# Kernel tuning notes

Hardware: AMD Instinct MI355X
Metric: run time of the kernel (lower is better)

## Reference

```python
import jax, jax.numpy as jnp
import numpy as np

PAD = 0
B, S, D, H, NH, PF, V, NMAX, L = 32, 512, 256, 512, 8, 2048, 100000, 15, 2
HD = H // NH


def setup_inputs() -> dict:
    key = jax.random.key(0)
    ks = iter(jax.random.split(key, 40))
    N = B * S
    p = lambda *s: jax.random.normal(next(ks), s, dtype=jnp.float32) * 0.02
    return dict(
        src=jax.random.randint(next(ks), (B, S), 0, V),
        src_lengths=jax.random.randint(next(ks), (B,), 1, S + 1),
        neighbor_idx=jax.random.randint(next(ks), (N, NMAX), 0, N),
        neighbor_count=jax.random.randint(next(ks), (N,), 0, NMAX + 1),
        time_intervals=jax.random.uniform(next(ks), (B, S), dtype=jnp.float32),
        emb=p(V, D).at[PAD].set(0.0),
        time_W=p(D), time_b=p(D),
        soc_W=p(D, D), soc_b=p(D), soc_g=jnp.ones(D), soc_beta=jnp.zeros(D),
        proj_W=p(D, H), proj_b=p(H),
        Wq=p(L, H, H), bq=p(L, H), Wk=p(L, H, H), bk=p(L, H),
        Wv=p(L, H, H), bv=p(L, H), Wo=p(L, H, H), bo=p(L, H),
        ln1_g=jnp.ones((L, H)), ln1_b=jnp.zeros((L, H)),
        ff_W1=p(L, H, PF), ff_b1=p(L, PF), ff_W2=p(L, PF, H), ff_b2=p(L, H),
        ln2_g=jnp.ones((L, H)), ln2_b=jnp.zeros((L, H)),
    )


def _ln(x, g, b):
    mu = x.mean(-1, keepdims=True)
    v = ((x - mu) ** 2).mean(-1, keepdims=True)
    return (x - mu) / jnp.sqrt(v + 1e-5) * g + b


def _forward(src, neighbor_idx, neighbor_count, time_intervals, emb, time_W, time_b,
             soc_W, soc_b, soc_g, soc_beta, proj_W, proj_b,
             Wq, bq, Wk, bk, Wv, bv, Wo, bo, ln1_g, ln1_b,
             ff_W1, ff_b1, ff_W2, ff_b2, ln2_g, ln2_b):
    # embedding + sinusoidal positional encoding
    x = emb[src]  # [B,S,D]
    pos = jnp.arange(S, dtype=jnp.float32)[:, None]
    div = jnp.exp(jnp.arange(0, D, 2, dtype=jnp.float32) * (-np.log(10000.0) / D))
    pe = jnp.zeros((S, D)).at[:, 0::2].set(jnp.sin(pos * div)).at[:, 1::2].set(jnp.cos(pos * div))
    x = x + pe
    # time interval encoding: Linear(1, D) on t[...,None]
    x = x + time_intervals[..., None] * time_W + time_b
    # neighbor aggregation (batched form of the per-node loop: mean over <=15 valid neighbors)
    N = B * S
    flat = x.reshape(N, D)
    nb = flat[neighbor_idx]  # [N, NMAX, D] irregular gather
    m = (jnp.arange(NMAX)[None, :] < neighbor_count[:, None]).astype(flat.dtype)
    agg = (nb * m[..., None]).sum(1) / jnp.maximum(neighbor_count, 1).astype(flat.dtype)[:, None]
    soc = jax.nn.relu(_ln(flat + agg @ soc_W + soc_b, soc_g, soc_beta))
    soc = jnp.where((neighbor_count > 0)[:, None], soc, flat)  # no neighbors -> passthrough
    soc = jnp.where((src.reshape(N) != PAD)[:, None], soc, 0.0)  # only valid (non-PAD) tokens
    x = x + 0.2 * soc.reshape(B, S, D)
    # transformer encoder stack
    h = x @ proj_W + proj_b
    kmask = src != PAD  # [B,S]
    for l in range(L):
        q = (h @ Wq[l] + bq[l]).reshape(B, S, NH, HD)
        k = (h @ Wk[l] + bk[l]).reshape(B, S, NH, HD)
        v = (h @ Wv[l] + bv[l]).reshape(B, S, NH, HD)
        e = jnp.einsum('bqhd,bkhd->bhqk', q, k) / jnp.sqrt(jnp.float32(HD))
        e = jnp.where(kmask[:, None, None, :], e, -1e10)
        a = jax.nn.softmax(e, axis=-1)
        o = jnp.einsum('bhqk,bkhd->bqhd', a, v).reshape(B, S, H)
        h = _ln(h + o @ Wo[l] + bo[l], ln1_g[l], ln1_b[l])
        ff = jax.nn.relu(h @ ff_W1[l] + ff_b1[l]) @ ff_W2[l] + ff_b2[l]
        h = _ln(h + ff, ln2_g[l], ln2_b[l])
    return h, x  # (src_out, embedded)


def reference(src, src_lengths, neighbor_idx, neighbor_count, time_intervals, emb, time_W, time_b,
              soc_W, soc_b, soc_g, soc_beta, proj_W, proj_b,
              Wq, bq, Wk, bk, Wv, bv, Wo, bo, ln1_g, ln1_b,
              ff_W1, ff_b1, ff_W2, ff_b2, ln2_g, ln2_b):
    # src_lengths unused by the original forward
    return _forward(src, neighbor_idx, neighbor_count, time_intervals, emb, time_W, time_b,
                    soc_W, soc_b, soc_g, soc_beta, proj_W, proj_b,
                    Wq, bq, Wk, bk, Wv, bv, Wo, bo, ln1_g, ln1_b,
                    ff_W1, ff_b1, ff_W2, ff_b2, ln2_g, ln2_b)
```

## Files before the change

### kernel.cpp

```cpp
#include <hip/hip_runtime.h>

#define BB 32
#define SS 512
#define DD 256
#define HHH 512
#define NHH 8
#define HDD 64
#define PFF 2048
#define LLL 2
#define NN (BB*SS)
#define NMAXX 15

typedef unsigned short u16;
typedef unsigned int u32;

typedef __attribute__((ext_vector_type(8))) __bf16 bf16x8;
typedef __attribute__((ext_vector_type(4))) float f32x4;

__device__ __forceinline__ float bf2f(u16 u) {
  union { u32 i; float f; } x; x.i = ((u32)u) << 16; return x.f;
}
__device__ __forceinline__ u16 f2bf(float f) {
  union { float f; u32 i; } x; x.f = f;
  u32 r = x.i + 0x7FFFu + ((x.i >> 16) & 1u);
  return (u16)(r >> 16);
}
__device__ __forceinline__ float ldf(const void* p, size_t i, int flag) {
  return flag ? bf2f(((const u16*)p)[i]) : ((const float*)p)[i];
}
__device__ __forceinline__ void stf(void* p, size_t i, int flag, float v) {
  if (flag) ((u16*)p)[i] = f2bf(v); else ((float*)p)[i] = v;
}
__device__ __forceinline__ void gld16(const u16* g, u16* l) {
  __builtin_amdgcn_global_load_lds(
      (const __attribute__((address_space(1))) u32*)g,
      (__attribute__((address_space(3))) u32*)l, 16, 0, 0);
}

__global__ void k_flag(const u32* __restrict__ ones, int* __restrict__ flag) {
  *flag = (ones[0] == 0x3F800000u) ? 0 : 1;
}

__global__ __launch_bounds__(256) void k_transpose_f(const void* __restrict__ in, size_t ioff,
    u16* __restrict__ out, int R, int C, const int* __restrict__ flagp) {
  __shared__ u16 tile[32][33];
  int flag = *flagp;
  int c0 = blockIdx.x * 32, r0 = blockIdx.y * 32;
  int tx = threadIdx.x, ty = threadIdx.y;
  #pragma unroll
  for (int i = 0; i < 4; ++i)
    tile[ty + i*8][tx] = f2bf(ldf(in, ioff + (size_t)(r0 + ty + i*8) * C + c0 + tx, flag));
  __syncthreads();
  #pragma unroll
  for (int i = 0; i < 4; ++i) out[(size_t)(c0 + ty + i*8) * R + r0 + tx] = tile[tx][ty + i*8];
}

__global__ __launch_bounds__(256) void k_packb(const void* __restrict__ projb,
    const void* __restrict__ bq, const void* __restrict__ bk, const void* __restrict__ bv,
    const void* __restrict__ b1, const void* __restrict__ bo, const void* __restrict__ b2,
    u16* __restrict__ out, const int* __restrict__ flagp) {
  int flag = *flagp;
  int i = blockIdx.x * 256 + threadIdx.x;
  int tot = 512 + LLL * 4608;
  if (i >= tot) return;
  float v;
  if (i < 512) v = ldf(projb, i, flag);
  else {
    int j = i - 512, l = j / 4608, r = j % 4608;
    if      (r < 512)  v = ldf(bq, (size_t)l * HHH + r, flag);
    else if (r < 1024) v = ldf(bk, (size_t)l * HHH + r - 512, flag);
    else if (r < 1536) v = ldf(bv, (size_t)l * HHH + r - 1024, flag);
    else if (r < 3584) v = ldf(b1, (size_t)l * PFF + r - 1536, flag);
    else if (r < 4096) v = ldf(bo, (size_t)l * HHH + r - 3584, flag);
    else               v = ldf(b2, (size_t)l * HHH + r - 4096, flag);
  }
  out[i] = f2bf(v);
}

__global__ __launch_bounds__(256) void k_pe(const void* __restrict__ tB,
    u16* __restrict__ pet, const int* __restrict__ flagp) {
  int flag = *flagp;
  int s = blockIdx.x, d = threadIdx.x;
  int i2 = d & ~1;
  float freq = expf(-0.035977892078031968f * (float)i2);
  float ang = (float)s * freq;
  float v = ((d & 1) ? cosf(ang) : sinf(ang)) + ldf(tB, d, flag);
  pet[(size_t)s * DD + d] = f2bf(v);
}

__global__ __launch_bounds__(256) void k_embed(const int* __restrict__ src,
    const void* __restrict__ tiv, const void* __restrict__ emb,
    const void* __restrict__ tW, const u16* __restrict__ pet,
    u16* __restrict__ X, const int* __restrict__ flagp) {
  int flag = *flagp;
  int n = blockIdx.x, d = threadIdx.x;
  int s = n & (SS - 1);
  int tok = src[n];
  float v = ldf(emb, (size_t)tok * DD + d, flag);
  v += bf2f(pet[(size_t)s * DD + d]);
  float t = ldf(tiv, n, flag);
  v += t * ldf(tW, d, flag);
  X[(size_t)n * DD + d] = f2bf(v);
}

__global__ __launch_bounds__(256) void k_agg(const int* __restrict__ nidx,
    const int* __restrict__ ncnt, const u16* __restrict__ X, u16* __restrict__ AGG) {
  int n = blockIdx.x, d = threadIdx.x;
  int cnt = ncnt[n];
  float s = 0.f;
  for (int j = 0; j < cnt; ++j) {
    int m = nidx[n * NMAXX + j];
    s += bf2f(X[(size_t)m * DD + d]);
  }
  float div = (float)(cnt > 0 ? cnt : 1);
  AGG[(size_t)n * DD + d] = f2bf(s / div);
}

__global__ __launch_bounds__(256) void k_gemm128(const u16* __restrict__ A,
    const u16* __restrict__ BT, const void* __restrict__ bias, int boff,
    const u16* __restrict__ res, u16* __restrict__ C, int N, int K, int relu,
    const int* __restrict__ flagp) {
  __shared__ __align__(16) u16 As[128 * 32];
  __shared__ __align__(16) u16 Bs[128 * 32];
  int n0 = blockIdx.x * 128, m0 = blockIdx.y * 128;
  int t = threadIdx.x;
  int lane = t & 63, w = t >> 6;
  int wm = (w >> 1) * 64, wn = (w & 1) * 64;
  int fr = lane & 15, fq = lane >> 4;
  int srow = t >> 2, sseg = t & 3;

  f32x4 acc[4][4];
  #pragma unroll
  for (int i = 0; i < 4; ++i)
    #pragma unroll
    for (int j = 0; j < 4; ++j) acc[i][j] = (f32x4){0.f, 0.f, 0.f, 0.f};

  const u16* ga = A  + (size_t)(m0 + srow) * K + sseg * 8;
  const u16* gb = BT + (size_t)(n0 + srow) * K + sseg * 8;
  u16* lA = As + srow * 32 + sseg * 8;
  u16* lB = Bs + srow * 32 + sseg * 8;
  const size_t rstride = (size_t)64 * K;

  for (int k0 = 0; k0 < K; k0 += 32) {
    gld16(ga + k0, lA);
    gld16(ga + k0 + rstride, lA + 64 * 32);
    gld16(gb + k0, lB);
    gld16(gb + k0 + rstride, lB + 64 * 32);
    __syncthreads();
    bf16x8 af[4], bf[4];
    #pragma unroll
    for (int i = 0; i < 4; ++i) af[i] = *(const bf16x8*)&As[(wm + i * 16 + fr) * 32 + fq * 8];
    #pragma unroll
    for (int j = 0; j < 4; ++j) bf[j] = *(const bf16x8*)&Bs[(wn + j * 16 + fr) * 32 + fq * 8];
    #pragma unroll
    for (int i = 0; i < 4; ++i)
      #pragma unroll
      for (int j = 0; j < 4; ++j)
        acc[i][j] = __builtin_amdgcn_mfma_f32_16x16x32_bf16(af[i], bf[j], acc[i][j], 0, 0, 0);
    __syncthreads();
  }

  int flag = *flagp;
  #pragma unroll
  for (int j = 0; j < 4; ++j) {
    int col = n0 + wn + j * 16 + fr;
    float bv = bias ? ldf(bias, boff + col, flag) : 0.f;
    #pragma unroll
    for (int i = 0; i < 4; ++i) {
      #pragma unroll
      for (int c = 0; c < 4; ++c) {
        int row = m0 + wm + i * 16 + fq * 4 + c;
        float v = acc[i][j][c] + bv;
        if (res) v += bf2f(res[(size_t)row * N + col]);
        if (relu) v = fmaxf(v, 0.f);
        C[(size_t)row * N + col] = f2bf(v);
      }
    }
  }
}

template<int NBF>
__global__ __launch_bounds__(512, 2) void k_gemm256(const u16* __restrict__ A,
    const u16* __restrict__ BT, const u16* __restrict__ bias,
    u16* __restrict__ C, int N, int K, int relu, int nbx) {
  constexpr int AG = 1024;
  constexpr int BG = NBF * 256;
  constexpr int STRIDE = (AG + BG) * 8;
  constexpr int LPT = 2 + BG / 512;
  __shared__ __align__(16) u16 S[3 * STRIDE];

  int nwg = gridDim.x;
  int id = blockIdx.x;
  int wg = ((nwg & 7) == 0) ? ((id & 7) * (nwg >> 3) + (id >> 3)) : id;
  int bx = wg % nbx, by = wg / nbx;
  int m0 = by * 256, n0 = bx * (64 * NBF);

  int t = threadIdx.x;
  int w = t >> 6, lane = t & 63;
  int fr = lane & 15, fq = lane >> 4;
  int wm = (w >> 2) * 128, wn = (w & 3) * (16 * NBF);
  int gsw8 = (fq ^ (fr & 3) ^ ((fr >> 2) & 3)) * 8;

  int arow = t >> 2, aseg = t & 3;
  int asw = aseg ^ (arow & 3) ^ ((arow >> 2) & 3);
  const u16* gA  = A  + (size_t)(m0 + arow) * K + asw * 8;
  const u16* gA2 = gA + (size_t)128 * K;
  const u16* gB  = BT + (size_t)(n0 + arow) * K + asw * 8;
  const u16* gB2 = gB + (size_t)128 * K;

  f32x4 acc[8][NBF];
  #pragma unroll
  for (int i = 0; i < 8; ++i)
    #pragma unroll
    for (int j = 0; j < NBF; ++j) acc[i][j] = (f32x4){0.f, 0.f, 0.f, 0.f};

  int NT = K >> 5;

  #pragma unroll
  for (int p = 0; p < 2; ++p) {
    gld16(gA  + p * 32, S + p * STRIDE + t * 8);
    gld16(gA2 + p * 32, S + p * STRIDE + (t + 512) * 8);
    gld16(gB  + p * 32, S + p * STRIDE + AG * 8 + t * 8);
    if constexpr (NBF == 4)
      gld16(gB2 + p * 32, S + p * STRIDE + AG * 8 + (t + 512) * 8);
  }
  asm volatile("s_waitcnt vmcnt(%0)" :: "n"(LPT) : "memory");
  __builtin_amdgcn_s_barrier();
  __builtin_amdgcn_sched_barrier(0);

  for (int T = 0; T < NT; ++T) {
    const u16* Sa = S + (T % 3) * STRIDE;
    const u16* Sb = Sa + AG * 8;
    u16* Sn = S + ((T + 2) % 3) * STRIDE;
    int kn = (T + 2) * 32;
    bool st = (T + 2) < NT;

    bf16x8 af[4], bf[NBF];
    #pragma unroll
    for (int i = 0; i < 4; ++i) af[i] = *(const bf16x8*)&Sa[(wm + i * 16 + fr) * 32 + gsw8];
    #pragma unroll
    for (int j = 0; j < NBF; ++j) bf[j] = *(const bf16x8*)&Sb[(wn + j * 16 + fr) * 32 + gsw8];
    if (st) {
      gld16(gA  + kn, Sn + t * 8);
      gld16(gA2 + kn, Sn + (t + 512) * 8);
    }
    __builtin_amdgcn_s_setprio(1);
    #pragma unroll
    for (int i = 0; i < 4; ++i)
      #pragma unroll
      for (int j = 0; j < NBF; ++j)
        acc[i][j] = __builtin_amdgcn_mfma_f32_16x16x32_bf16(af[i], bf[j], acc[i][j], 0, 0, 0);
    __builtin_amdgcn_s_setprio(0);

    bf16x8 ag[4];
    #pragma unroll
    for (int i = 0; i < 4; ++i) ag[i] = *(const bf16x8*)&Sa[(wm + 64 + i * 16 + fr) * 32 + gsw8];
    if (st) {
      gld16(gB + kn, Sn + AG * 8 + t * 8);
      if constexpr (NBF == 4)
        gld16(gB2 + kn, Sn + AG * 8 + (t + 512) * 8);
    }
    __builtin_amdgcn_s_setprio(1);
    #pragma unroll
    for (int i = 0; i < 4; ++i)
      #pragma unroll
      for (int j = 0; j < NBF; ++j)
        acc[4 + i][j] = __builtin_amdgcn_mfma_f32_16x16x32_bf16(ag[i], bf[j], acc[4 + i][j], 0, 0, 0);
    __builtin_amdgcn_s_setprio(0);

    if (st) { asm volatile("s_waitcnt vmcnt(%0) lgkmcnt(0)" :: "n"(LPT) : "memory"); }
    else    { asm volatile("s_waitcnt vmcnt(0) lgkmcnt(0)" ::: "memory"); }
    __builtin_amdgcn_s_barrier();
    __builtin_amdgcn_sched_barrier(0);
  }

  float bvj[NBF];
  #pragma unroll
  for (int j = 0; j < NBF; ++j) bvj[j] = bf2f(bias[n0 + wn + j * 16 + fr]);
  #pragma unroll
  for (int i = 0; i < 8; ++i) {
    #pragma unroll
    for (int c = 0; c < 4; ++c) {
      size_t rowb = (size_t)(m0 + wm + i * 16 + fq * 4 + c) * N;
      #pragma unroll
      for (int j = 0; j < NBF; ++j) {
        int col = n0 + wn + j * 16 + fr;
        float v = acc[i][j][c] + bvj[j];
        if (relu) v = fmaxf(v, 0.f);
        C[rowb + col] = f2bf(v);
      }
    }
  }
}

__global__ __launch_bounds__(256) void k_ln_soc(const u16* __restrict__ socp,
    const u16* __restrict__ X, const void* __restrict__ g, const void* __restrict__ beta,
    const int* __restrict__ ncnt, const int* __restrict__ src,
    u16* __restrict__ X2, void* __restrict__ dout, const int* __restrict__ flagp) {
  __shared__ float sred[4];
  int flag = *flagp;
  int n = blockIdx.x, t = threadIdx.x;
  size_t base = (size_t)n * DD;
  float v = bf2f(socp[base + t]);
  float s = v;
  #pragma unroll
  for (int o = 32; o; o >>= 1) s += __shfl_xor(s, o, 64);
  if ((t & 63) == 0) sred[t >> 6] = s;
  __syncthreads();
  float mean = (sred[0] + sred[1] + sred[2] + sred[3]) * (1.f / DD);
  float dv = v - mean;
  float q = dv * dv;
  #pragma unroll
  for (int o = 32; o; o >>= 1) q += __shfl_xor(q, o, 64);
  __syncthreads();
  if ((t & 63) == 0) sred[t >> 6] = q;
  __syncthreads();
  float var = (sred[0] + sred[1] + sred[2] + sred[3]) * (1.f / DD);
  float rs = rsqrtf(var + 1e-5f);
  float soc = fmaxf(dv * rs * ldf(g, t, flag) + ldf(beta, t, flag), 0.f);
  float xv = bf2f(X[base + t]);
  if (ncnt[n] <= 0) soc = xv;
  if (src[n] == 0)  soc = 0.f;
  float ov = xv + 0.2f * soc;
  X2[base + t] = f2bf(ov);
  stf(dout, (size_t)NN * HHH + base + t, flag, ov);
}

__global__ __launch_bounds__(256) void k_ln_add(const u16* __restrict__ a,
    const u16* __restrict__ b, const void* __restrict__ g, int goff,
    const void* __restrict__ bb, int boff, u16* __restrict__ out,
    void* __restrict__ dout, const int* __restrict__ flagp) {
  __shared__ float sred[4];
  int flag = *flagp;
  int row = blockIdx.x, t = threadIdx.x;
  size_t base = (size_t)row * HHH;
  float v0 = bf2f(a[base + t])       + bf2f(b[base + t]);
  float v1 = bf2f(a[base + 256 + t]) + bf2f(b[base + 256 + t]);
  float s = v0 + v1;
  #pragma unroll
  for (int o = 32; o; o >>= 1) s += __shfl_xor(s, o, 64);
  if ((t & 63) == 0) sred[t >> 6] = s;
  __syncthreads();
  float mean = (sred[0] + sred[1] + sred[2] + sred[3]) * (1.f / HHH);
  float d0 = v0 - mean, d1 = v1 - mean;
  float q = d0 * d0 + d1 * d1;
  #pragma unroll
  for (int o = 32; o; o >>= 1) q += __shfl_xor(q, o, 64);
  __syncthreads();
  if ((t & 63) == 0) sred[t >> 6] = q;
  __syncthreads();
  float var = (sred[0] + sred[1] + sred[2] + sred[3]) * (1.f / HHH);
  float rs = rsqrtf(var + 1e-5f);
  float o0 = d0 * rs * ldf(g, goff + t, flag)       + ldf(bb, boff + t, flag);
  float o1 = d1 * rs * ldf(g, goff + 256 + t, flag) + ldf(bb, boff + 256 + t, flag);
  if (dout) {
    stf(dout, base + t, flag, o0);
    stf(dout, base + 256 + t, flag, o1);
  } else {
    out[base + t]       = f2bf(o0);
    out[base + 256 + t] = f2bf(o1);
  }
}

__global__ __launch_bounds__(512, 2) void k_attn_mfma(const u16* __restrict__ Q,
    const u16* __restrict__ Kb, const u16* __restrict__ Vb, int ld,
    const int* __restrict__ src, u16* __restrict__ O) {
  __shared__ __align__(16) u16 Ks[512 * 64];
  __shared__ __align__(16) u16 VTs[64 * 512];
  __shared__ __align__(16) u16 Ps[128 * 72];
  __shared__ float maskv[512];
  int h = blockIdx.x, b = blockIdx.y;
  int t = threadIdx.x;
  int w = t >> 6, lane = t & 63;
  int fr = lane & 15, fq = lane >> 4;

  maskv[t] = (src[b * SS + t] != 0) ? 1.f : 0.f;

  #pragma unroll
  for (int i = 0; i < 8; ++i) {
    int off = t + i * 512;
    int row = off >> 3;
    int gs  = (off & 7) ^ (row & 7);
    gld16(Kb + (size_t)(b * SS + row) * ld + h * HDD + gs * 8, Ks + (size_t)off * 8);
  }
  {
    const u16* vsrc = Vb + (size_t)(b * SS + t) * ld + h * HDD;
    int ghi = (t >> 3) & ~7, glo = (t >> 3) & 7, kw = t & 7;
    #pragma unroll
    for (int i = 0; i < 8; ++i) {
      uint4 raw = *(const uint4*)(vsrc + i * 8);
      u16 e[8]; *(uint4*)e = raw;
      #pragma unroll
      for (int jj = 0; jj < 8; ++jj) {
        int d = i * 8 + jj;
        VTs[(size_t)d * 512 + (size_t)((ghi | (glo ^ (d & 7))) * 8 + kw)] = e[jj];
      }
    }
  }
  __syncthreads();

  for (int chunk = 0; chunk < 4; ++chunk) {
    int qb = chunk * 128 + w * 16;
    bf16x8 qf[2];
    #pragma unroll
    for (int kc = 0; kc < 2; ++kc)
      qf[kc] = *(const bf16x8*)&Q[(size_t)(b * SS + qb + fr) * ld + h * HDD + kc * 32 + fq * 8];

    f32x4 sacc[32];
    #pragma unroll
    for (int j = 0; j < 32; ++j) sacc[j] = (f32x4){0.f, 0.f, 0.f, 0.f};

    #pragma unroll
    for (int kt = 0; kt < 32; ++kt) {
      int row = kt * 16 + fr;
      #pragma unroll
      for (int kc = 0; kc < 2; ++kc) {
        bf16x8 kf = *(const bf16x8*)&Ks[(size_t)row * 64 +
            (size_t)(((kc * 4 + fq) ^ (fr & 7)) * 8)];
        sacc[kt] = __builtin_amdgcn_mfma_f32_16x16x32_bf16(qf[kc], kf, sacc[kt], 0, 0, 0);
      }
    }

    #pragma unroll
    for (int j = 0; j < 32; ++j) {
      float mv = maskv[j * 16 + fr];
      #pragma unroll
      for (int c = 0; c < 4; ++c) {
        float v = sacc[j][c] * 0.125f;
        sacc[j][c] = (mv != 0.f) ? v : -1e10f;
      }
    }
    #pragma unroll
    for (int c = 0; c < 4; ++c) {
      float m = -3.0e38f;
      #pragma unroll
      for (int j = 0; j < 32; ++j) m = fmaxf(m, sacc[j][c]);
      #pragma unroll
      for (int o = 1; o < 16; o <<= 1) m = fmaxf(m, __shfl_xor(m, o, 64));
      float s = 0.f;
      #pragma unroll
      for (int j = 0; j < 32; ++j) { float e = __expf(sacc[j][c] - m); sacc[j][c] = e; s += e; }
      #pragma unroll
      for (int o = 1; o < 16; o <<= 1) s += __shfl_xor(s, o, 64);
      float inv = 1.f / s;
      #pragma unroll
      for (int j = 0; j < 32; ++j) sacc[j][c] *= inv;
    }

    f32x4 oacc[4];
    #pragma unroll
    for (int n = 0; n < 4; ++n) oacc[n] = (f32x4){0.f, 0.f, 0.f, 0.f};

    #pragma unroll
    for (int seg = 0; seg < 8; ++seg) {
      #pragma unroll
      for (int tt = 0; tt < 4; ++tt)
        #pragma unroll
        for (int c = 0; c < 4; ++c)
          Ps[(size_t)(w * 16 + fq * 4 + c) * 72 + tt * 16 + fr] = f2bf(sacc[seg * 4 + tt][c]);
      #pragma unroll
      for (int kc = 0; kc < 2; ++kc) {
        bf16x8 pa = *(const bf16x8*)&Ps[(size_t)(w * 16 + fr) * 72 + kc * 32 + fq * 8];
        #pragma unroll
        for (int nt = 0; nt < 4; ++nt) {
          bf16x8 bv = *(const bf16x8*)&VTs[(size_t)(nt * 16 + fr) * 512 +
              (size_t)((seg * 8 + ((kc * 4 + fq) ^ (fr & 7))) * 8)];
          oacc[nt] = __builtin_amdgcn_mfma_f32_16x16x32_bf16(pa, bv, oacc[nt], 0, 0, 0);
        }
      }
    }

    #pragma unroll
    for (int nt = 0; nt < 4; ++nt)
      #pragma unroll
      for (int c = 0; c < 4; ++c)
        O[(size_t)(b * SS + qb + fq * 4 + c) * HHH + h * HDD + nt * 16 + fr] = f2bf(oacc[nt][c]);
  }
}

extern "C" void kernel_launch(void* const* d_in, const int* in_sizes, int n_in,
                              void* d_out, int out_size, void* d_ws, size_t ws_size,
                              hipStream_t stream) {
  (void)in_sizes; (void)n_in; (void)out_size;
  const int* src    = (const int*)d_in[0];
  const int* nidx   = (const int*)d_in[2];
  const int* ncnt   = (const int*)d_in[3];
  const void* tiv   = d_in[4];
  const void* emb   = d_in[5];
  const void* tW    = d_in[6];
  const void* tB    = d_in[7];
  const void* socW  = d_in[8];
  const void* socb  = d_in[9];
  const void* socg  = d_in[10];
  const void* socbe = d_in[11];
  const void* projW = d_in[12];
  const void* projb = d_in[13];
  const void* Wq    = d_in[14];
  const void* bq    = d_in[15];
  const void* Wk    = d_in[16];
  const void* bk    = d_in[17];
  const void* Wv    = d_in[18];
  const void* bv    = d_in[19];
  const void* Wo    = d_in[20];
  const void* bo    = d_in[21];
  const void* ln1g  = d_in[22];
  const void* ln1b  = d_in[23];
  const void* W1    = d_in[24];
  const void* b1    = d_in[25];
  const void* W2    = d_in[26];
  const void* b2    = d_in[27];
  const void* ln2g  = d_in[28];
  const void* ln2b  = d_in[29];

  const size_t NHS = (size_t)NN * HHH;
  const size_t QKV3 = (size_t)3 * HHH * HHH;
  u16* ws = (u16*)d_ws;
  u16* socWT  = ws;
  u16* projWT = socWT + (size_t)DD * DD;
  u16* WqkvT  = projWT + (size_t)DD * HHH;
  u16* WoT    = WqkvT + (size_t)LLL * QKV3;
  u16* W1T    = WoT + (size_t)LLL * HHH * HHH;
  u16* W2T    = W1T + (size_t)LLL * HHH * PFF;
  u16* Hb     = W2T + (size_t)LLL * HHH * PFF;
  u16* P1     = Hb + NHS;
  u16* P2     = P1 + NHS;
  u16* P3     = P2 + NHS;
  int* flagp  = (int*)(P3 + NHS);
  u16* packb  = (u16*)(flagp + 4);
  u16* pet    = packb + 16384;
  u16* FFMf   = pet + (size_t)SS * DD;
  size_t need_full = (size_t)(FFMf - ws + (size_t)NN * PFF) * 2;
  int fullff = (ws_size >= need_full);

  u16* X    = P1;
  u16* AGG  = P2;
  u16* SOCP = P3;
  u16* X2   = P2;
  u16* Ob   = (u16*)d_out;
  u16* FFMc = P2;

  k_flag<<<1, 1, 0, stream>>>((const u32*)ln1g, flagp);

  dim3 tb(32, 8);
  k_transpose_f<<<dim3(DD / 32, DD / 32), tb, 0, stream>>>(socW, 0, socWT, DD, DD, flagp);
  k_transpose_f<<<dim3(HHH / 32, DD / 32), tb, 0, stream>>>(projW, 0, projWT, DD, HHH, flagp);
  for (int l = 0; l < LLL; ++l) {
    size_t oHH = (size_t)l * HHH * HHH, oHP = (size_t)l * HHH * PFF;
    u16* wq = WqkvT + (size_t)l * QKV3;
    k_transpose_f<<<dim3(HHH / 32, HHH / 32), tb, 0, stream>>>(Wq, oHH, wq, HHH, HHH, flagp);
    k_transpose_f<<<dim3(HHH / 32, HHH / 32), tb, 0, stream>>>(Wk, oHH, wq + (size_t)HHH * HHH, HHH, HHH, flagp);
    k_transpose_f<<<dim3(HHH / 32, HHH / 32), tb, 0, stream>>>(Wv, oHH, wq + (size_t)2 * HHH * HHH, HHH, HHH, flagp);
    k_transpose_f<<<dim3(HHH / 32, HHH / 32), tb, 0, stream>>>(Wo, oHH, WoT + oHH, HHH, HHH, flagp);
    k_transpose_f<<<dim3(PFF / 32, HHH / 32), tb, 0, stream>>>(W1, oHP, W1T + oHP, HHH, PFF, flagp);
    k_transpose_f<<<dim3(HHH / 32, PFF / 32), tb, 0, stream>>>(W2, oHP, W2T + oHP, PFF, HHH, flagp);
  }
  k_packb<<<dim3((512 + LLL * 4608 + 255) / 256), 256, 0, stream>>>(
      projb, bq, bk, bv, b1, bo, b2, packb, flagp);
  k_pe<<<SS, 256, 0, stream>>>(tB, pet, flagp);

  k_embed<<<NN, 256, 0, stream>>>(src, tiv, emb, tW, pet, X, flagp);
  k_agg<<<NN, 256, 0, stream>>>(nidx, ncnt, X, AGG);
  k_gemm128<<<dim3(DD / 128, NN / 128), 256, 0, stream>>>(AGG, socWT, socb, 0, X, SOCP, DD, DD, 0, flagp);
  k_ln_soc<<<NN, 256, 0, stream>>>(SOCP, X, socg, socbe, ncnt, src, X2, d_out, flagp);
  k_gemm256<2><<<dim3(256), 512, 0, stream>>>(X2, projWT, packb, Hb, HHH, DD, 0, 4);

  for (int l = 0; l < LLL; ++l) {
    size_t oHH = (size_t)l * HHH * HHH, oHP = (size_t)l * HHH * PFF;
    u16* lb = packb + 512 + (size_t)l * 4608;
    k_gemm256<4><<<dim3(384), 512, 0, stream>>>(Hb, WqkvT + (size_t)l * QKV3, lb, P1, 1536, HHH, 0, 6);
    k_attn_mfma<<<dim3(NHH, BB), 512, 0, stream>>>(P1, P1 + HHH, P1 + 2 * HHH, 3 * HHH, src, Ob);
    k_gemm256<2><<<dim3(256), 512, 0, stream>>>(Ob, WoT + oHH, lb + 3584, P1, HHH, HHH, 0, 4);
    k_ln_add<<<NN, 256, 0, stream>>>(Hb, P1, ln1g, l * HHH, ln1b, l * HHH, Hb, nullptr, flagp);
    if (fullff) {
      k_gemm256<4><<<dim3(512), 512, 0, stream>>>(Hb, W1T + oHP, lb + 1536, FFMf, PFF, HHH, 1, 8);
      k_gemm256<2><<<dim3(256), 512, 0, stream>>>(FFMf, W2T + oHP, lb + 4096, P1, HHH, PFF, 0, 4);
    } else {
      for (int c = 0; c < 2; ++c) {
        const u16* Asrc = Hb + (size_t)c * 8192 * HHH;
        u16* Cdst = P1 + (size_t)c * 8192 * HHH;
        k_gemm256<4><<<dim3(256), 512, 0, stream>>>(Asrc, W1T + oHP, lb + 1536, FFMc, PFF, HHH, 1, 8);
        k_gemm256<2><<<dim3(128), 512, 0, stream>>>(FFMc, W2T + oHP, lb + 4096, Cdst, HHH, PFF, 0, 4);
      }
    }
    void* dd = (l == LLL - 1) ? d_out : nullptr;
    k_ln_add<<<NN, 256, 0, stream>>>(Hb, P1, ln2g, l * HHH, ln2b, l * HHH, Hb, dd, flagp);
  }
}
```

Measured before the change: 804.5 us.

## Merge weight transposes into one launch and streamline attention softmax

The fourteen per-matrix transpose launches become one kernel that maps block IDs to the right weight matrix, cutting launch overhead. In attention, the MFMA operands are swapped so each lane holds scores for a full row segment. The mask becomes an additive bias loaded as a vector, and the max and sum reductions need two cross-lane shuffles instead of several per column. Normalisation is deferred to the output store, and P is packed to bf16 with v_cvt_pk_bf16_f32 using 8-byte LDS writes. The risk is subtle numerical differences from the additive mask and the deferred scaling.

```diff
diff --git a/kernel.cpp b/kernel.cpp
--- a/kernel.cpp
+++ b/kernel.cpp
@@ -41,11 +41,34 @@
   *flag = (ones[0] == 0x3F800000u) ? 0 : 1;
 }
 
-__global__ __launch_bounds__(256) void k_transpose_f(const void* __restrict__ in, size_t ioff,
-    u16* __restrict__ out, int R, int C, const int* __restrict__ flagp) {
+__global__ __launch_bounds__(256) void k_transpose_all(
+    const void* __restrict__ socW, const void* __restrict__ projW,
+    const void* __restrict__ Wq, const void* __restrict__ Wk,
+    const void* __restrict__ Wv, const void* __restrict__ Wo,
+    const void* __restrict__ W1, const void* __restrict__ W2,
+    u16* __restrict__ socWT, u16* __restrict__ projWT, u16* __restrict__ WqkvT,
+    u16* __restrict__ WoT, u16* __restrict__ W1T, u16* __restrict__ W2T,
+    const int* __restrict__ flagp) {
+  const size_t HH2 = (size_t)HHH * HHH, HP = (size_t)HHH * PFF;
+  int bid = blockIdx.x;
+  const void* in; size_t ioff; u16* out; int R, C;
+  if (bid < 64)       { in = socW;  ioff = 0; out = socWT;  R = DD; C = DD;  }
+  else if (bid < 192) { bid -= 64; in = projW; ioff = 0; out = projWT; R = DD; C = HHH; }
+  else {
+    int r = bid - 192;
+    int l = r / 3072; r -= l * 3072;
+    size_t oHH = (size_t)l * HH2, oHP = (size_t)l * HP;
+    if (r < 256)       { in = Wq; ioff = oHH; out = WqkvT + (size_t)l*3*HH2;          R = HHH; C = HHH; bid = r; }
+    else if (r < 512)  { in = Wk; ioff = oHH; out = WqkvT + (size_t)l*3*HH2 + HH2;    R = HHH; C = HHH; bid = r - 256; }
+    else if (r < 768)  { in = Wv; ioff = oHH; out = WqkvT + (size_t)l*3*HH2 + 2*HH2;  R = HHH; C = HHH; bid = r - 512; }
+    else if (r < 1024) { in = Wo; ioff = oHH; out = WoT + oHH;                        R = HHH; C = HHH; bid = r - 768; }
+    else if (r < 2048) { in = W1; ioff = oHP; out = W1T + oHP;                        R = HHH; C = PFF; bid = r - 1024; }
+    else               { in = W2; ioff = oHP; out = W2T + oHP;                        R = PFF; C = HHH; bid = r - 2048; }
+  }
+  int ntx = C >> 5;
+  int c0 = (bid % ntx) * 32, r0 = (bid / ntx) * 32;
   __shared__ u16 tile[32][33];
   int flag = *flagp;
-  int c0 = blockIdx.x * 32, r0 = blockIdx.y * 32;
   int tx = threadIdx.x, ty = threadIdx.y;
   #pragma unroll
   for (int i = 0; i < 4; ++i)
@@ -368,13 +391,13 @@
   __shared__ __align__(16) u16 Ks[512 * 64];
   __shared__ __align__(16) u16 VTs[64 * 512];
   __shared__ __align__(16) u16 Ps[128 * 72];
-  __shared__ float maskv[512];
+  __shared__ __align__(16) float maskv[512];
   int h = blockIdx.x, b = blockIdx.y;
   int t = threadIdx.x;
   int w = t >> 6, lane = t & 63;
   int fr = lane & 15, fq = lane >> 4;
 
-  maskv[t] = (src[b * SS + t] != 0) ? 1.f : 0.f;
+  maskv[t] = (src[b * SS + t] != 0) ? 0.f : -8.0e10f;
 
   #pragma unroll
   for (int i = 0; i < 8; ++i) {
@@ -417,47 +440,60 @@
       for (int kc = 0; kc < 2; ++kc) {
         bf16x8 kf = *(const bf16x8*)&Ks[(size_t)row * 64 +
             (size_t)(((kc * 4 + fq) ^ (fr & 7)) * 8)];
-        sacc[kt] = __builtin_amdgcn_mfma_f32_16x16x32_bf16(qf[kc], kf, sacc[kt], 0, 0, 0);
+        sacc[kt] = __builtin_amdgcn_mfma_f32_16x16x32_bf16(kf, qf[kc], sacc[kt], 0, 0, 0);
       }
     }
 
     #pragma unroll
     for (int j = 0; j < 32; ++j) {
-      float mv = maskv[j * 16 + fr];
-      #pragma unroll
-      for (int c = 0; c < 4; ++c) {
-        float v = sacc[j][c] * 0.125f;
-        sacc[j][c] = (mv != 0.f) ? v : -1e10f;
+      f32x4 av = *(const f32x4*)&maskv[j * 16 + fq * 4];
+      #pragma unroll
+      for (int c = 0; c < 4; ++c) sacc[j][c] += av[c];
+    }
+
+    float m0 = -3.0e38f, m1 = -3.0e38f, m2 = -3.0e38f, m3 = -3.0e38f;
+    #pragma unroll
+    for (int j = 0; j < 32; ++j) {
+      m0 = fmaxf(m0, sacc[j][0]); m1 = fmaxf(m1, sacc[j][1]);
+      m2 = fmaxf(m2, sacc[j][2]); m3 = fmaxf(m3, sacc[j][3]);
+    }
+    float m = fmaxf(fmaxf(m0, m1), fmaxf(m2, m3));
+    m = fmaxf(m, __shfl_xor(m, 16, 64));
+    m = fmaxf(m, __shfl_xor(m, 32, 64));
+    float ms = m * 0.125f;
+    float s0 = 0.f, s1 = 0.f, s2 = 0.f, s3 = 0.f;
+    #pragma unroll
+    for (int j = 0; j < 32; ++j) {
+      float e0 = __expf(fmaf(sacc[j][0], 0.125f, -ms));
+      float e1 = __expf(fmaf(sacc[j][1], 0.125f, -ms));
+      float e2 = __expf(fmaf(sacc[j][2], 0.125f, -ms));
+      float e3 = __expf(fmaf(sacc[j][3], 0.125f, -ms));
+      sacc[j][0] = e0; sacc[j][1] = e1; sacc[j][2] = e2; sacc[j][3] = e3;
+      s0 += e0; s1 += e1; s2 += e2; s3 += e3;
+    }
+    float s = (s0 + s1) + (s2 + s3);
+    s += __shfl_xor(s, 16, 64);
+    s += __shfl_xor(s, 32, 64);
+    float inv = 1.f / s;
+    float invc[4];
+    #pragma unroll
+    for (int c = 0; c < 4; ++c) invc[c] = __shfl(inv, fq * 4 + c, 64);
+
+    f32x4 oacc[4];
+    #pragma unroll
+    for (int n = 0; n < 4; ++n) oacc[n] = (f32x4){0.f, 0.f, 0.f, 0.f};
+
+    #pragma unroll
+    for (int seg = 0; seg < 8; ++seg) {
+      #pragma unroll
+      for (int tt = 0; tt < 4; ++tt) {
+        int j = seg * 4 + tt;
+        u32 lo, hi;
+        asm("v_cvt_pk_bf16_f32 %0, %1, %2" : "=v"(lo) : "v"(sacc[j][0]), "v"(sacc[j][1]));
+        asm("v_cvt_pk_bf16_f32 %0, %1, %2" : "=v"(hi) : "v"(sacc[j][2]), "v"(sacc[j][3]));
+        uint2 pk; pk.x = lo; pk.y = hi;
+        *(uint2*)&Ps[(size_t)(w * 16 + fr) * 72 + tt * 16 + fq * 4] = pk;
       }
-    }
-    #pragma unroll
-    for (int c = 0; c < 4; ++c) {
-      float m = -3.0e38f;
-      #pragma unroll
-      for (int j = 0; j < 32; ++j) m = fmaxf(m, sacc[j][c]);
-      #pragma unroll
-      for (int o = 1; o < 16; o <<= 1) m = fmaxf(m, __shfl_xor(m, o, 64));
-      float s = 0.f;
-      #pragma unroll
-      for (int j = 0; j < 32; ++j) { float e = __expf(sacc[j][c] - m); sacc[j][c] = e; s += e; }
-      #pragma unroll
-      for (int o = 1; o < 16; o <<= 1) s += __shfl_xor(s, o, 64);
-      float inv = 1.f / s;
-      #pragma unroll
-      for (int j = 0; j < 32; ++j) sacc[j][c] *= inv;
-    }
-
-    f32x4 oacc[4];
-    #pragma unroll
-    for (int n = 0; n < 4; ++n) oacc[n] = (f32x4){0.f, 0.f, 0.f, 0.f};
-
-    #pragma unroll
-    for (int seg = 0; seg < 8; ++seg) {
-      #pragma unroll
-      for (int tt = 0; tt < 4; ++tt)
-        #pragma unroll
-        for (int c = 0; c < 4; ++c)
-          Ps[(size_t)(w * 16 + fq * 4 + c) * 72 + tt * 16 + fr] = f2bf(sacc[seg * 4 + tt][c]);
       #pragma unroll
       for (int kc = 0; kc < 2; ++kc) {
         bf16x8 pa = *(const bf16x8*)&Ps[(size_t)(w * 16 + fr) * 72 + kc * 32 + fq * 8];
@@ -474,7 +510,8 @@
     for (int nt = 0; nt < 4; ++nt)
       #pragma unroll
       for (int c = 0; c < 4; ++c)
-        O[(size_t)(b * SS + qb + fq * 4 + c) * HHH + h * HDD + nt * 16 + fr] = f2bf(oacc[nt][c]);
+        O[(size_t)(b * SS + qb + fq * 4 + c) * HHH + h * HDD + nt * 16 + fr] =
+            f2bf(oacc[nt][c] * invc[c]);
   }
 }
 
@@ -542,18 +579,9 @@
   k_flag<<<1, 1, 0, stream>>>((const u32*)ln1g, flagp);
 
   dim3 tb(32, 8);
-  k_transpose_f<<<dim3(DD / 32, DD / 32), tb, 0, stream>>>(socW, 0, socWT, DD, DD, flagp);
-  k_transpose_f<<<dim3(HHH / 32, DD / 32), tb, 0, stream>>>(projW, 0, projWT, DD, HHH, flagp);
-  for (int l = 0; l < LLL; ++l) {
-    size_t oHH = (size_t)l * HHH * HHH, oHP = (size_t)l * HHH * PFF;
-    u16* wq = WqkvT + (size_t)l * QKV3;
-    k_transpose_f<<<dim3(HHH / 32, HHH / 32), tb, 0, stream>>>(Wq, oHH, wq, HHH, HHH, flagp);
-    k_transpose_f<<<dim3(HHH / 32, HHH / 32), tb, 0, stream>>>(Wk, oHH, wq + (size_t)HHH * HHH, HHH, HHH, flagp);
-    k_transpose_f<<<dim3(HHH / 32, HHH / 32), tb, 0, stream>>>(Wv, oHH, wq + (size_t)2 * HHH * HHH, HHH, HHH, flagp);
-    k_transpose_f<<<dim3(HHH / 32, HHH / 32), tb, 0, stream>>>(Wo, oHH, WoT + oHH, HHH, HHH, flagp);
-    k_transpose_f<<<dim3(PFF / 32, HHH / 32), tb, 0, stream>>>(W1, oHP, W1T + oHP, HHH, PFF, flagp);
-    k_transpose_f<<<dim3(HHH / 32, PFF / 32), tb, 0, stream>>>(W2, oHP, W2T + oHP, PFF, HHH, flagp);
-  }
+  k_transpose_all<<<dim3(192 + LLL * 3072), tb, 0, stream>>>(
+      socW, projW, Wq, Wk, Wv, Wo, W1, W2,
+      socWT, projWT, WqkvT, WoT, W1T, W2T, flagp);
   k_packb<<<dim3((512 + LLL * 4608 + 255) / 256), 256, 0, stream>>>(
       projb, bq, bk, bv, b1, bo, b2, packb, flagp);
   k_pe<<<SS, 256, 0, stream>>>(tB, pet, flagp);
```

Result: slower. 1.101 ms (+36.8%).
